# Kernel optimization log

Measured on AMD Instinct MI355X. Metric: run time of the kernel, lower is better.

Reference implementation:

```python
import jax, jax.numpy as jnp
import numpy as np

N = 50000   # nodes per graph
E = 500000  # edges per graph
F_IN = 128  # num_features
H = 128     # hidden_channels
C = 64      # num_classes
G = 64      # graphs per batch
NEG_SLOPE = 0.2


def setup_inputs() -> dict:
    key = jax.random.key(0)
    ks = jax.random.split(key, 16)
    s = 1.0 / np.sqrt(H)
    return {
        "x1": jax.random.normal(ks[0], (N, F_IN), jnp.float32),
        "x2": jax.random.normal(ks[1], (N, F_IN), jnp.float32),
        # stacked params for the 2 GATConv layers (F_IN == H so shapes match)
        "convW": jax.random.normal(ks[2], (2, H, H), jnp.float32) * s,
        "att_src": jax.random.normal(ks[3], (2, H), jnp.float32) * s,
        "att_dst": jax.random.normal(ks[4], (2, H), jnp.float32) * s,
        "conv_b": jnp.zeros((2, H), jnp.float32),
        "mlp_w1": jax.random.normal(ks[5], (H, H), jnp.float32) * s,
        "mlp_b1": jnp.zeros((H,), jnp.float32),
        "mlp_w2": jax.random.normal(ks[6], (H, C), jnp.float32) * s,
        "mlp_b2": jnp.zeros((C,), jnp.float32),
        "edge_index1": jax.random.randint(ks[7], (2, E), 0, N, jnp.int64),
        "batch1": jnp.sort(jax.random.randint(ks[8], (N,), 0, G, jnp.int64)),
        "edge_index2": jax.random.randint(ks[9], (2, E), 0, N, jnp.int64),
        "batch2": jnp.sort(jax.random.randint(ks[10], (N,), 0, G, jnp.int64)),
    }


def gat_conv(x, src, dst, W, a_s, a_d, b):
    # PyG GATConv, heads=1, add_self_loops already applied in src/dst
    n = x.shape[0]
    h = x @ W                                   # [N, H]
    alpha_s = h @ a_s                           # [N]
    alpha_d = h @ a_d                           # [N]
    e = alpha_s[src] + alpha_d[dst]             # [Etot]
    e = jnp.where(e > 0, e, NEG_SLOPE * e)      # leaky_relu
    # segment softmax over incoming edges of each dst node
    m = jax.ops.segment_max(e, dst, num_segments=n)
    ex = jnp.exp(e - m[dst])
    denom = jax.ops.segment_sum(ex, dst, num_segments=n)
    alpha = ex / denom[dst]                     # [Etot]
    out = jax.ops.segment_sum(h[src] * alpha[:, None], dst, num_segments=n)
    return out + b


def reference(x1, x2, convW, att_src, att_dst, conv_b,
              mlp_w1, mlp_b1, mlp_w2, mlp_b2,
              edge_index1, batch1, edge_index2, batch2):
    def branch(x, ei):
        n = x.shape[0]
        loops = jnp.arange(n, dtype=ei.dtype)
        src = jnp.concatenate([ei[0], loops])
        dst = jnp.concatenate([ei[1], loops])
        # num_layers=3 -> 2 convs; i != num_layers-1 always true -> ELU after each
        for l in range(2):
            x = gat_conv(x, src, dst, convW[l], att_src[l], att_dst[l], conv_b[l])
            x = jax.nn.elu(x)
            # dropout p=0.5 is identity in eval mode
        return jax.nn.relu(x @ mlp_w1 + mlp_b1) @ mlp_w2 + mlp_b2

    h1 = branch(x1, edge_index1)
    h2 = branch(x2, edge_index2)
    p1 = jax.ops.segment_sum(h1, batch1, num_segments=G)  # [G, C]
    p2 = jax.ops.segment_sum(h2, batch2, num_segments=G)  # [G, C]
    return p1.T @ p2                                      # [C, C]
```

## Files before the change

### kernel.cpp

```cpp
#include <hip/hip_runtime.h>
#include <cstdint>
#include <cstddef>

#define NNODES 50000
#define NEDGES 500000
#define NTOT (NEDGES + NNODES)
#define HDIM 128
#define CDIM 64
#define GDIM 64
#define NB 250
#define NPB 200
#define CHUNK 2048
#define NCHB ((NEDGES + CHUNK - 1) / CHUNK)

typedef __bf16 bf16x8 __attribute__((ext_vector_type(8)));
typedef __bf16 bf16x2 __attribute__((ext_vector_type(2)));
typedef float f32x4 __attribute__((ext_vector_type(4)));


__global__ __launch_bounds__(256) void k_setup(const float* __restrict__ convW,
                                               const float* __restrict__ w1,
                                               const float* __restrict__ w2,
                                               const float* __restrict__ a_s,
                                               const float* __restrict__ a_d,
                                               __bf16* __restrict__ WtC,
                                               __bf16* __restrict__ Wt1,
                                               __bf16* __restrict__ Wt2,
                                               float* __restrict__ Wa,
                                               float* __restrict__ p) {
    int b = blockIdx.x, tid = threadIdx.x;
    if (b < 128) {
        int i = b * 256 + tid;
        int mat = i >> 14, rem = i & 16383;
        int k = rem >> 7, n = rem & 127;
        WtC[mat * 16384 + n * 128 + k] = (__bf16)convW[i];
    } else if (b < 192) {
        int i = (b - 128) * 256 + tid;
        int k = i >> 7, n = i & 127;
        Wt1[n * 128 + k] = (__bf16)w1[i];
    } else if (b < 224) {
        int i = (b - 192) * 256 + tid;
        int k = i >> 6, n = i & 63;
        Wt2[n * 128 + k] = (__bf16)w2[i];
    } else if (b == 224) {
        for (int o = tid; o < 512; o += 256) {
            int l = o >> 8, r = o & 255;
            int type = r >> 7, k = r & 127;
            const float* a = (type ? a_d : a_s) + l * 128;
            const float* Wrow = convW + l * 16384 + k * 128;
            float s = 0.f;
            for (int j = 0; j < 128; j++) s += Wrow[j] * a[j];
            Wa[o] = s;
        }
    } else {
        for (int i = tid; i < 2 * GDIM * CDIM; i += 256) p[i] = 0.f;
    }
}


__global__ __launch_bounds__(256) void k_bhist(const int* __restrict__ ei0,
                                               const int* __restrict__ ei1,
                                               int* __restrict__ bcntB, int e) {
    __shared__ int h[NB];
    const int* dst = (blockIdx.y ? ei1 : ei0) + NEDGES;
    int* bcnt = bcntB + blockIdx.y * NB;
    for (int t = threadIdx.x; t < NB; t += 256) h[t] = 0;
    __syncthreads();
    int base = blockIdx.x * CHUNK;
    int lim = min(base + CHUNK, e);
    for (int i = base + threadIdx.x; i < lim; i += 256) atomicAdd(&h[dst[i] / NPB], 1);
    __syncthreads();
    for (int t = threadIdx.x; t < NB; t += 256)
        if (h[t]) atomicAdd(&bcnt[t], h[t]);
}

__global__ __launch_bounds__(256) void k_bscan(const int* __restrict__ bcntB,
                                               int* __restrict__ boffB,
                                               int* __restrict__ bcurB) {
    __shared__ int s[256];
    int t = threadIdx.x;
    const int* bcnt = bcntB + blockIdx.y * NB;
    int* boff = boffB + blockIdx.y * (NB + 1);
    int* bcur = bcurB + blockIdx.y * NB;
    int v = (t < NB) ? bcnt[t] : 0;
    s[t] = v;
    __syncthreads();
    for (int off = 1; off < 256; off <<= 1) {
        int x = (t >= off) ? s[t - off] : 0;
        __syncthreads();
        s[t] += x;
        __syncthreads();
    }
    if (t < NB) {
        boff[t + 1] = s[t];
        bcur[t] = s[t] - v;
        if (t == 0) boff[0] = 0;
    }
}

__global__ __launch_bounds__(256) void k_part(const int* __restrict__ ei0,
                                              const int* __restrict__ ei1,
                                              int* __restrict__ bcurB,
                                              int2* __restrict__ partB, int e) {
    __shared__ int cnt[NB], boffL[NB], gbase[NB], cur2[NB];
    __shared__ int tmp[256];
    __shared__ int2 staged[CHUNK];
    const int* eis = blockIdx.y ? ei1 : ei0;
    int* bcur = bcurB + blockIdx.y * NB;
    int2* part = partB + blockIdx.y * (size_t)NEDGES;
    int t = threadIdx.x;
    for (int i = t; i < NB; i += 256) { cnt[i] = 0; cur2[i] = 0; }
    __syncthreads();
    int base = blockIdx.x * CHUNK;
    int lim = min(base + CHUNK, e);
    int nloc = lim - base;

    int s_[8], d_[8], b_[8];
    bool v_[8];
#pragma unroll
    for (int k = 0; k < 8; k++) {
        int i = base + k * 256 + t;
        v_[k] = i < lim;
        s_[k] = 0; d_[k] = 0; b_[k] = 0;
        if (v_[k]) {
            s_[k] = eis[i];
            d_[k] = eis[NEDGES + i];
            b_[k] = d_[k] / NPB;
            atomicAdd(&cnt[b_[k]], 1);
        }
    }
    __syncthreads();
    tmp[t] = (t < NB) ? cnt[t] : 0;
    __syncthreads();
    for (int off = 1; off < 256; off <<= 1) {
        int x = (t >= off) ? tmp[t - off] : 0;
        __syncthreads();
        tmp[t] += x;
        __syncthreads();
    }
    if (t < NB) boffL[t] = tmp[t] - cnt[t];
    __syncthreads();
    if (t < NB) {
        int c = cnt[t];
        gbase[t] = c ? atomicAdd(&bcur[t], c) : 0;
    }
    __syncthreads();
#pragma unroll
    for (int k = 0; k < 8; k++) {
        if (v_[k]) {
            int pos = atomicAdd(&cur2[b_[k]], 1);
            staged[boffL[b_[k]] + pos] = make_int2(s_[k], d_[k]);
        }
    }
    __syncthreads();
    for (int i = t; i < nloc; i += 256) {
        int2 r = staged[i];
        int b = r.y / NPB;
        part[gbase[b] + (i - boffL[b])] = r;
    }
}

__global__ __launch_bounds__(256) void k_place(const int2* __restrict__ partB,
                                               const int* __restrict__ boffB,
                                               int* __restrict__ rpB, size_t sNp1,
                                               int* __restrict__ colB, size_t sE) {
    __shared__ int h[NPB];
    __shared__ int lds4[4];
    int b = blockIdx.x;
    const int* boff = boffB + blockIdx.y * (NB + 1);
    const int2* part = partB + blockIdx.y * (size_t)NEDGES;
    int* row_ptr = rpB + blockIdx.y * sNp1;
    int* col = colB + blockIdx.y * sE;
    int t = threadIdx.x;
    int n0 = b * NPB;
    if (t < NPB) h[t] = 0;
    __syncthreads();
    int beg = boff[b], end = boff[b + 1];
    for (int i = beg + t; i < end; i += 256) atomicAdd(&h[part[i].y - n0], 1);
    __syncthreads();
    int v = (t < NPB) ? h[t] : 0;
    int lane = t & 63, wid = t >> 6;
    int incl = v;
#pragma unroll
    for (int off = 1; off < 64; off <<= 1) {
        int nv = __shfl_up(incl, off);
        if (lane >= off) incl += nv;
    }
    if (lane == 63) lds4[wid] = incl;
    __syncthreads();
    if (t == 0) {
        int s = 0;
#pragma unroll
        for (int j = 0; j < 4; j++) { s += lds4[j]; lds4[j] = s; }
    }
    __syncthreads();
    if (wid > 0) incl += lds4[wid - 1];
    if (t < NPB) {
        int rp_end = beg + n0 + incl + t + 1;
        row_ptr[n0 + t + 1] = rp_end;
        int rp_start = rp_end - v - 1;
        col[rp_start] = n0 + t;
        h[t] = rp_start + 1;
        if (b == 0 && t == 0) row_ptr[0] = 0;
    }
    __syncthreads();
    for (int i = beg + t; i < end; i += 256) {
        int2 r = part[i];
        int p = atomicAdd(&h[r.y - n0], 1);
        col[p] = r.x;
    }
}


template <bool AF32>
__global__ __launch_bounds__(256) void k_gemm_conv(const float* __restrict__ x0,
                                                   const float* __restrict__ x1,
                                                   const __bf16* __restrict__ Ab, size_t As_,
                                                   const __bf16* __restrict__ Wt,
                                                   const float* __restrict__ Was,
                                                   const float* __restrict__ Wad,
                                                   float* __restrict__ asB, float* __restrict__ adB,
                                                   size_t aS,
                                                   __bf16* __restrict__ OutB, size_t Os_, int M) {
    constexpr int BN = 128;
    __shared__ __align__(16) unsigned short As[64][136];
    __shared__ __align__(16) unsigned short Bs[BN][136];
    const int tid = threadIdx.x;
    const int lane = tid & 63, w = tid >> 6;
    const int row0 = blockIdx.x * 64;
    __bf16* Out = OutB + blockIdx.y * Os_;

#pragma unroll
    for (int t = 0; t < 4; t++) {
        int ch = t * 256 + tid;
        int r = ch >> 4, cx = ch & 15;
        int grow = row0 + r;
        bf16x8 v = {};
        if (grow < M) {
            if (AF32) {
                const float* Ap = (blockIdx.y ? x1 : x0) + (size_t)grow * 128 + cx * 8;
                float4 f0 = *reinterpret_cast<const float4*>(Ap);
                float4 f1 = *reinterpret_cast<const float4*>(Ap + 4);
                v[0] = (__bf16)f0.x; v[1] = (__bf16)f0.y; v[2] = (__bf16)f0.z; v[3] = (__bf16)f0.w;
                v[4] = (__bf16)f1.x; v[5] = (__bf16)f1.y; v[6] = (__bf16)f1.z; v[7] = (__bf16)f1.w;
            } else {
                v = *reinterpret_cast<const bf16x8*>(Ab + blockIdx.y * As_ + (size_t)grow * 128 + cx * 8);
            }
        }
        *reinterpret_cast<bf16x8*>(&As[r][cx * 8]) = v;
    }
#pragma unroll
    for (int t = 0; t < 8; t++) {
        int ch = t * 256 + tid;
        int r = ch >> 4, cx = ch & 15;
        bf16x8 v = *reinterpret_cast<const bf16x8*>(Wt + (size_t)r * 128 + cx * 8);
        *reinterpret_cast<bf16x8*>(&Bs[r][cx * 8]) = v;
    }
    __syncthreads();

    {
        int row = tid >> 2, seg = tid & 3;
        float ss = 0.f, sd = 0.f;
#pragma unroll
        for (int k = 0; k < 32; k++) {
            int kk = seg * 32 + k;
            float a = __int_as_float(((unsigned)As[row][kk]) << 16);
            ss += a * Was[kk];
            sd += a * Wad[kk];
        }
        ss += __shfl_xor(ss, 1); ss += __shfl_xor(ss, 2);
        sd += __shfl_xor(sd, 1); sd += __shfl_xor(sd, 2);
        if (seg == 0) {
            int grow = row0 + row;
            if (grow < M) {
                (asB + blockIdx.y * aS)[grow] = ss;
                (adB + blockIdx.y * aS)[grow] = sd;
            }
        }
    }

    const int wr0 = (w >> 1) * 32;
    const int wc0 = (w & 1) * 64;
    f32x4 acc[2][4] = {};

#pragma unroll
    for (int ks = 0; ks < 4; ks++) {
        const int koff = ks * 32 + (lane >> 4) * 8;
        bf16x8 af[2], bfr[4];
#pragma unroll
        for (int mf = 0; mf < 2; mf++)
            af[mf] = *reinterpret_cast<const bf16x8*>(&As[wr0 + mf * 16 + (lane & 15)][koff]);
#pragma unroll
        for (int nf = 0; nf < 4; nf++)
            bfr[nf] = *reinterpret_cast<const bf16x8*>(&Bs[wc0 + nf * 16 + (lane & 15)][koff]);
#pragma unroll
        for (int mf = 0; mf < 2; mf++)
#pragma unroll
            for (int nf = 0; nf < 4; nf++)
                acc[mf][nf] = __builtin_amdgcn_mfma_f32_16x16x32_bf16(af[mf], bfr[nf], acc[mf][nf], 0, 0, 0);
    }

#pragma unroll
    for (int mf = 0; mf < 2; mf++) {
#pragma unroll
        for (int r = 0; r < 4; r++) {
            int row = row0 + wr0 + mf * 16 + (lane >> 4) * 4 + r;
            if (row >= M) continue;
#pragma unroll
            for (int nf = 0; nf < 4; nf++) {
                int colc = wc0 + nf * 16 + (lane & 15);
                Out[(size_t)row * BN + colc] = (__bf16)acc[mf][nf][r];
            }
        }
    }
}


__global__ __launch_bounds__(256) void k_gat_agg(const __bf16* __restrict__ hB, size_t hS,
                                                 const float* __restrict__ asB,
                                                 const float* __restrict__ adB, size_t aS,
                                                 const int* __restrict__ rpB, size_t sNp1,
                                                 const int* __restrict__ colB, size_t sE,
                                                 const float* __restrict__ bias,
                                                 __bf16* __restrict__ outB, size_t oS, int n) {
    int grp = threadIdx.x >> 4;
    int node = blockIdx.x * 16 + grp;
    int l = threadIdx.x & 15;
    if (node >= n) return;
    const float* alpha_s = asB + blockIdx.y * aS;
    const int* row_ptr = rpB + blockIdx.y * sNp1;
    const int* col = colB + blockIdx.y * sE;
    const char* hbase = (const char*)(hB + blockIdx.y * hS);
    float ad = (adB + blockIdx.y * aS)[node];
    int beg = row_ptr[node], end = row_ptr[node + 1];
    int deg = end - beg;
    int foff = l * 16;

    float acc[8] = {0.f, 0.f, 0.f, 0.f, 0.f, 0.f, 0.f, 0.f};

    if (deg <= 16) {
        bool v = l < deg;
        int c = 0;
        float e = -1e30f;
        if (v) {
            c = col[beg + l];
            float t = alpha_s[c] + ad;
            e = (t > 0.f) ? t : 0.2f * t;
        }
        float m = e;
#pragma unroll
        for (int off = 8; off; off >>= 1) m = fmaxf(m, __shfl_xor(m, off));
        float ex = v ? __expf(e - m) : 0.f;
        float den = ex;
#pragma unroll
        for (int off = 8; off; off >>= 1) den += __shfl_xor(den, off);
        float wn = ex / den;

        int base = (grp << 4) & 63;
        for (int e2 = 0; e2 < deg; e2 += 2) {
            int i1 = base + e2, i2 = base + e2 + 1;
            int s1 = __shfl(c, i1); float w1 = __shfl(wn, i1);
            int s2 = __shfl(c, i2); float w2 = __shfl(wn, i2);
            bool h2v = (e2 + 1) < deg;
            s2 = h2v ? s2 : s1;
            w2 = h2v ? w2 : 0.f;
            bf16x8 h1 = *reinterpret_cast<const bf16x8*>(hbase + ((size_t)(unsigned)s1 << 8) + foff);
            bf16x8 hh2 = *reinterpret_cast<const bf16x8*>(hbase + ((size_t)(unsigned)s2 << 8) + foff);
#pragma unroll
            for (int q = 0; q < 8; q++) acc[q] += w1 * (float)h1[q] + w2 * (float)hh2[q];
        }
    } else {
        float m = -1e30f;
        for (int i = beg + l; i < end; i += 16) {
            float t = alpha_s[col[i]] + ad;
            t = (t > 0.f) ? t : 0.2f * t;
            m = fmaxf(m, t);
        }
#pragma unroll
        for (int off = 8; off; off >>= 1) m = fmaxf(m, __shfl_xor(m, off));
        float den = 0.f;
        for (int i = beg + l; i < end; i += 16) {
            float t = alpha_s[col[i]] + ad;
            t = (t > 0.f) ? t : 0.2f * t;
            den += __expf(t - m);
        }
#pragma unroll
        for (int off = 8; off; off >>= 1) den += __shfl_xor(den, off);
        float rinv = 1.f / den;
        for (int e2 = beg; e2 < end; e2++) {
            int cc = col[e2];
            float t = alpha_s[cc] + ad;
            t = (t > 0.f) ? t : 0.2f * t;
            float wv = __expf(t - m) * rinv;
            bf16x8 hv = *reinterpret_cast<const bf16x8*>(hbase + ((size_t)(unsigned)cc << 8) + foff);
#pragma unroll
            for (int q = 0; q < 8; q++) acc[q] += wv * (float)hv[q];
        }
    }

    float4 b0 = *reinterpret_cast<const float4*>(bias + l * 8);
    float4 b1 = *reinterpret_cast<const float4*>(bias + l * 8 + 4);
    float bb[8] = {b0.x, b0.y, b0.z, b0.w, b1.x, b1.y, b1.z, b1.w};
    bf16x8 o;
#pragma unroll
    for (int q = 0; q < 8; q++) {
        float x = acc[q] + bb[q];
        x = (x > 0.f) ? x : __expf(x) - 1.f;
        o[q] = (__bf16)x;
    }
    *reinterpret_cast<bf16x8*>((char*)(outB + blockIdx.y * oS) + ((size_t)(unsigned)node << 8) + foff) = o;
}


__global__ __launch_bounds__(256) void k_mlp_pool(const __bf16* __restrict__ AbB, size_t As_,
                                                  const __bf16* __restrict__ Wt1,
                                                  const __bf16* __restrict__ Wt2,
                                                  const float* __restrict__ b1,
                                                  const float* __restrict__ b2,
                                                  const int* __restrict__ bat0,
                                                  const int* __restrict__ bat1,
                                                  float* __restrict__ pB, size_t pS, int M) {
    __shared__ __align__(16) unsigned short As[64][136];
    __shared__ __align__(16) unsigned short Bs[128][136];
    const int tid = threadIdx.x;
    const int lane = tid & 63, w = tid >> 6;
    const int row0 = blockIdx.x * 64;
    const __bf16* Ab = AbB + blockIdx.y * As_;
    const int* batch = blockIdx.y ? bat1 : bat0;
    float* p = pB + blockIdx.y * pS;

#pragma unroll
    for (int t = 0; t < 4; t++) {
        int ch = t * 256 + tid;
        int r = ch >> 4, cx = ch & 15;
        int grow = row0 + r;
        bf16x8 v = {};
        if (grow < M) v = *reinterpret_cast<const bf16x8*>(Ab + (size_t)grow * 128 + cx * 8);
        *reinterpret_cast<bf16x8*>(&As[r][cx * 8]) = v;
    }
#pragma unroll
    for (int t = 0; t < 8; t++) {
        int ch = t * 256 + tid;
        int r = ch >> 4, cx = ch & 15;
        bf16x8 v = *reinterpret_cast<const bf16x8*>(Wt1 + (size_t)r * 128 + cx * 8);
        *reinterpret_cast<bf16x8*>(&Bs[r][cx * 8]) = v;
    }
    __syncthreads();

    {
        const int wr0 = (w >> 1) * 32;
        const int wc0 = (w & 1) * 64;
        f32x4 acc[2][4] = {};
#pragma unroll
        for (int ks = 0; ks < 4; ks++) {
            const int koff = ks * 32 + (lane >> 4) * 8;
            bf16x8 af[2], bfr[4];
#pragma unroll
            for (int mf = 0; mf < 2; mf++)
                af[mf] = *reinterpret_cast<const bf16x8*>(&As[wr0 + mf * 16 + (lane & 15)][koff]);
#pragma unroll
            for (int nf = 0; nf < 4; nf++)
                bfr[nf] = *reinterpret_cast<const bf16x8*>(&Bs[wc0 + nf * 16 + (lane & 15)][koff]);
#pragma unroll
            for (int mf = 0; mf < 2; mf++)
#pragma unroll
                for (int nf = 0; nf < 4; nf++)
                    acc[mf][nf] = __builtin_amdgcn_mfma_f32_16x16x32_bf16(af[mf], bfr[nf], acc[mf][nf], 0, 0, 0);
        }
        __syncthreads();
#pragma unroll
        for (int mf = 0; mf < 2; mf++)
#pragma unroll
            for (int r = 0; r < 4; r++) {
                int row = wr0 + mf * 16 + (lane >> 4) * 4 + r;
#pragma unroll
                for (int nf = 0; nf < 4; nf++) {
                    int colc = wc0 + nf * 16 + (lane & 15);
                    float v = fmaxf(acc[mf][nf][r] + b1[colc], 0.f);
                    As[row][colc] = __builtin_bit_cast(unsigned short, (__bf16)v);
                }
            }
#pragma unroll
        for (int t = 0; t < 4; t++) {
            int ch = t * 256 + tid;
            int r = ch >> 4, cx = ch & 15;
            bf16x8 v = *reinterpret_cast<const bf16x8*>(Wt2 + (size_t)r * 128 + cx * 8);
            *reinterpret_cast<bf16x8*>(&Bs[r][cx * 8]) = v;
        }
        __syncthreads();
    }

    const int wr2 = w * 16;
    f32x4 acc2[4] = {};
#pragma unroll
    for (int ks = 0; ks < 4; ks++) {
        const int koff = ks * 32 + (lane >> 4) * 8;
        bf16x8 a2 = *reinterpret_cast<const bf16x8*>(&As[wr2 + (lane & 15)][koff]);
#pragma unroll
        for (int nf = 0; nf < 4; nf++) {
            bf16x8 bf2 = *reinterpret_cast<const bf16x8*>(&Bs[nf * 16 + (lane & 15)][koff]);
            acc2[nf] = __builtin_amdgcn_mfma_f32_16x16x32_bf16(a2, bf2, acc2[nf], 0, 0, 0);
        }
    }

    int q = lane >> 4, c = lane & 15;
    bool full = (row0 + 63) < M;
    int g0 = batch[min(row0, M - 1)];
    int g1 = batch[min(row0 + 63, M - 1)];
    if (full && g0 == g1) {
        float s0 = acc2[0][0] + acc2[0][1] + acc2[0][2] + acc2[0][3];
        float s1 = acc2[1][0] + acc2[1][1] + acc2[1][2] + acc2[1][3];
        float s2 = acc2[2][0] + acc2[2][1] + acc2[2][2] + acc2[2][3];
        float s3 = acc2[3][0] + acc2[3][1] + acc2[3][2] + acc2[3][3];
        s0 += __shfl_xor(s0, 16); s0 += __shfl_xor(s0, 32);
        s1 += __shfl_xor(s1, 16); s1 += __shfl_xor(s1, 32);
        s2 += __shfl_xor(s2, 16); s2 += __shfl_xor(s2, 32);
        s3 += __shfl_xor(s3, 16); s3 += __shfl_xor(s3, 32);
        float v = (q & 2) ? ((q & 1) ? s3 : s2) : ((q & 1) ? s1 : s0);
        v += 16.f * b2[q * 16 + c];
        atomicAdd(&p[g0 * CDIM + q * 16 + c], v);
    } else {
        float b2v[4];
#pragma unroll
        for (int nf = 0; nf < 4; nf++) b2v[nf] = b2[nf * 16 + c];
#pragma unroll
        for (int r = 0; r < 4; r++) {
            int row = row0 + wr2 + q * 4 + r;
            if (row >= M) continue;
            int g = batch[row];
#pragma unroll
            for (int nf = 0; nf < 4; nf++)
                atomicAdd(&p[g * CDIM + nf * 16 + c], acc2[nf][r] + b2v[nf]);
        }
    }
}


__global__ __launch_bounds__(64) void k_final(const float* __restrict__ p, float* __restrict__ out) {
    int i = blockIdx.x;
    int j = threadIdx.x;
    const float* p1 = p;
    const float* p2 = p + GDIM * CDIM;
    float s = 0.f;
    for (int g = 0; g < GDIM; ++g) s += p1[g * CDIM + i] * p2[g * CDIM + j];
    out[i * CDIM + j] = s;
}


static inline size_t align_up(size_t x, size_t a) { return (x + a - 1) & ~(a - 1); }

struct Ws {
    __bf16 *Hb, *Yb;
    __bf16 *WtC, *Wt1, *Wt2;
    float *alpha_s, *alpha_d, *Wa, *p;
    int *row_ptr, *col;
    int *bcnt, *boff, *bcur;
    int2* part;
    size_t sNH, sN, sNp1, sE;
    size_t need;
};

static Ws carve(void* ws, bool combined) {
    char* p = (char*)ws;
    size_t off = 0;
    Ws w;
    int nb = combined ? 2 : 1;
    auto take = [&](size_t bytes) {
        char* r = p + off;
        off = align_up(off + bytes, 256);
        return r;
    };
    w.Hb = (__bf16*)take((size_t)nb * NNODES * HDIM * 2);
    w.Yb = (__bf16*)take((size_t)nb * NNODES * HDIM * 2);
    w.alpha_s = (float*)take((size_t)nb * NNODES * 4);
    w.alpha_d = (float*)take((size_t)nb * NNODES * 4);
    w.col = (int*)take((size_t)nb * NTOT * 4);
    w.part = (int2*)take((size_t)nb * NEDGES * 8);
    w.row_ptr = (int*)take((size_t)nb * (NNODES + 1) * 4);
    w.bcnt = (int*)take((size_t)2 * NB * 4);
    w.boff = (int*)take((size_t)2 * (NB + 1) * 4);
    w.bcur = (int*)take((size_t)2 * NB * 4);
    w.WtC = (__bf16*)take((size_t)2 * HDIM * HDIM * 2);
    w.Wt1 = (__bf16*)take((size_t)HDIM * HDIM * 2);
    w.Wt2 = (__bf16*)take((size_t)HDIM * CDIM * 2);
    w.Wa = (float*)take((size_t)512 * 4);
    w.p = (float*)take((size_t)2 * GDIM * CDIM * 4);
    w.need = off;
    size_t s = combined ? 1 : 0;
    w.sNH = s * (size_t)NNODES * HDIM;
    w.sN = s * (size_t)NNODES;
    w.sNp1 = s * (size_t)(NNODES + 1);
    w.sE = s * (size_t)NTOT;
    return w;
}

static void pipeline(const Ws& w, const float* xA, const float* xB,
                     const int* eiA, const int* eiB,
                     const int* batA, const int* batB,
                     const float* conv_b, const float* b1, const float* b2,
                     float* pbase, size_t pstride, int yc, hipStream_t stream) {
    const int N = NNODES, E = NEDGES;
    dim3 gC(NCHB, yc), gB(NB, yc), g1(1, yc);
    dim3 gW((N + 15) / 16, yc);
    dim3 gG((N + 63) / 64, yc);

    hipMemsetAsync(w.bcnt, 0, (size_t)yc * NB * 4, stream);
    k_bhist<<<gC, 256, 0, stream>>>(eiA, eiB, w.bcnt, E);
    k_bscan<<<g1, 256, 0, stream>>>(w.bcnt, w.boff, w.bcur);
    k_part<<<gC, 256, 0, stream>>>(eiA, eiB, w.bcur, w.part, E);
    k_place<<<gB, 256, 0, stream>>>(w.part, w.boff, w.row_ptr, w.sNp1, w.col, w.sE);

    k_gemm_conv<true><<<gG, 256, 0, stream>>>(
        xA, xB, nullptr, 0, w.WtC, w.Wa, w.Wa + 128,
        w.alpha_s, w.alpha_d, w.sN, w.Hb, w.sNH, N);
    k_gat_agg<<<gW, 256, 0, stream>>>(w.Hb, w.sNH, w.alpha_s, w.alpha_d, w.sN,
                                      w.row_ptr, w.sNp1, w.col, w.sE, conv_b, w.Yb, w.sNH, N);
    k_gemm_conv<false><<<gG, 256, 0, stream>>>(
        nullptr, nullptr, w.Yb, w.sNH, w.WtC + HDIM * HDIM, w.Wa + 256, w.Wa + 384,
        w.alpha_s, w.alpha_d, w.sN, w.Hb, w.sNH, N);
    k_gat_agg<<<gW, 256, 0, stream>>>(w.Hb, w.sNH, w.alpha_s, w.alpha_d, w.sN,
                                      w.row_ptr, w.sNp1, w.col, w.sE, conv_b + HDIM, w.Yb, w.sNH, N);
    k_mlp_pool<<<gG, 256, 0, stream>>>(w.Yb, w.sNH, w.Wt1, w.Wt2, b1, b2,
                                       batA, batB, pbase, pstride, N);
}

extern "C" void kernel_launch(void* const* d_in, const int* in_sizes, int n_in, void* d_out,
                              int out_size, void* d_ws, size_t ws_size, hipStream_t stream) {
    const float* x1      = (const float*)d_in[0];
    const float* x2      = (const float*)d_in[1];
    const float* convW   = (const float*)d_in[2];
    const float* att_src = (const float*)d_in[3];
    const float* att_dst = (const float*)d_in[4];
    const float* conv_b  = (const float*)d_in[5];
    const float* mlp_w1  = (const float*)d_in[6];
    const float* mlp_b1  = (const float*)d_in[7];
    const float* mlp_w2  = (const float*)d_in[8];
    const float* mlp_b2  = (const float*)d_in[9];
    const int* ei1       = (const int*)d_in[10];
    const int* batch1    = (const int*)d_in[11];
    const int* ei2       = (const int*)d_in[12];
    const int* batch2    = (const int*)d_in[13];
    float* out = (float*)d_out;

    Ws wc = carve(d_ws, true);
    bool combined = ws_size >= wc.need;
    Ws w = combined ? wc : carve(d_ws, false);

    k_setup<<<226, 256, 0, stream>>>(convW, mlp_w1, mlp_w2, att_src, att_dst,
                                     w.WtC, w.Wt1, w.Wt2, w.Wa, w.p);

    if (combined) {
        pipeline(w, x1, x2, ei1, ei2, batch1, batch2, conv_b,
                 mlp_b1, mlp_b2, w.p, (size_t)GDIM * CDIM, 2, stream);
    } else {
        pipeline(w, x1, x1, ei1, ei1, batch1, batch1, conv_b,
                 mlp_b1, mlp_b2, w.p, 0, 1, stream);
        pipeline(w, x2, x2, ei2, ei2, batch2, batch2, conv_b,
                 mlp_b1, mlp_b2, w.p + GDIM * CDIM, 0, 1, stream);
    }

    k_final<<<CDIM, 64, 0, stream>>>(w.p, out);
}
```

Measured before the change: 346.9 us.

## Fuse pipeline into a persistent cooperative megakernel and pack partitioned edges

```diff
diff --git a/kernel.cpp b/kernel.cpp
--- a/kernel.cpp
+++ b/kernel.cpp
@@ -1,6 +1,9 @@
 #include <hip/hip_runtime.h>
+#include <hip/hip_cooperative_groups.h>
 #include <cstdint>
 #include <cstddef>
+
+namespace cg = cooperative_groups;
 
 #define NNODES 50000
 #define NEDGES 500000
@@ -12,76 +15,80 @@
 #define NPB 200
 #define CHUNK 2048
 #define NCHB ((NEDGES + CHUNK - 1) / CHUNK)
+#define SNH ((size_t)NNODES * HDIM)
+#define SN ((size_t)NNODES)
+#define SNP1 ((size_t)(NNODES + 1))
+#define SE ((size_t)NTOT)
+#define GEMM_TILES ((NNODES + 63) / 64)
+#define AGG_UNITS (NNODES / 16)
 
 typedef __bf16 bf16x8 __attribute__((ext_vector_type(8)));
 typedef __bf16 bf16x2 __attribute__((ext_vector_type(2)));
 typedef float f32x4 __attribute__((ext_vector_type(4)));
-
-
-__global__ __launch_bounds__(256) void k_setup(const float* __restrict__ convW,
-                                               const float* __restrict__ w1,
-                                               const float* __restrict__ w2,
-                                               const float* __restrict__ a_s,
-                                               const float* __restrict__ a_d,
-                                               __bf16* __restrict__ WtC,
-                                               __bf16* __restrict__ Wt1,
-                                               __bf16* __restrict__ Wt2,
-                                               float* __restrict__ Wa,
-                                               float* __restrict__ p) {
-    int b = blockIdx.x, tid = threadIdx.x;
+typedef unsigned short ushort_t;
+
+struct MegaArgs {
+    const float *x0, *x1, *convW, *att_s, *att_d, *conv_b, *w1, *b1, *w2, *b2;
+    const int *ei0, *ei1, *bat0, *bat1;
+    __bf16 *Hb, *Yb, *WtC, *Wt1, *Wt2;
+    float *alpha_s, *alpha_d, *Wa, *p;
+    int *row_ptr, *col, *bcnt, *boff, *bcur;
+    unsigned int* part;
+    float* out;
+    int nblk;
+};
+
+
+__device__ void d_setup(int b, int tid, const MegaArgs& A) {
     if (b < 128) {
         int i = b * 256 + tid;
         int mat = i >> 14, rem = i & 16383;
         int k = rem >> 7, n = rem & 127;
-        WtC[mat * 16384 + n * 128 + k] = (__bf16)convW[i];
+        A.WtC[mat * 16384 + n * 128 + k] = (__bf16)A.convW[i];
     } else if (b < 192) {
         int i = (b - 128) * 256 + tid;
         int k = i >> 7, n = i & 127;
-        Wt1[n * 128 + k] = (__bf16)w1[i];
+        A.Wt1[n * 128 + k] = (__bf16)A.w1[i];
     } else if (b < 224) {
         int i = (b - 192) * 256 + tid;
         int k = i >> 6, n = i & 63;
-        Wt2[n * 128 + k] = (__bf16)w2[i];
+        A.Wt2[n * 128 + k] = (__bf16)A.w2[i];
     } else if (b == 224) {
         for (int o = tid; o < 512; o += 256) {
             int l = o >> 8, r = o & 255;
             int type = r >> 7, k = r & 127;
-            const float* a = (type ? a_d : a_s) + l * 128;
-            const float* Wrow = convW + l * 16384 + k * 128;
+            const float* a = (type ? A.att_d : A.att_s) + l * 128;
+            const float* Wrow = A.convW + l * 16384 + k * 128;
             float s = 0.f;
             for (int j = 0; j < 128; j++) s += Wrow[j] * a[j];
-            Wa[o] = s;
+            A.Wa[o] = s;
         }
     } else {
-        for (int i = tid; i < 2 * GDIM * CDIM; i += 256) p[i] = 0.f;
-    }
-}
-
-
-__global__ __launch_bounds__(256) void k_bhist(const int* __restrict__ ei0,
-                                               const int* __restrict__ ei1,
-                                               int* __restrict__ bcntB, int e) {
-    __shared__ int h[NB];
-    const int* dst = (blockIdx.y ? ei1 : ei0) + NEDGES;
-    int* bcnt = bcntB + blockIdx.y * NB;
-    for (int t = threadIdx.x; t < NB; t += 256) h[t] = 0;
-    __syncthreads();
-    int base = blockIdx.x * CHUNK;
-    int lim = min(base + CHUNK, e);
-    for (int i = base + threadIdx.x; i < lim; i += 256) atomicAdd(&h[dst[i] / NPB], 1);
-    __syncthreads();
-    for (int t = threadIdx.x; t < NB; t += 256)
+        for (int i = tid; i < 2 * GDIM * CDIM; i += 256) A.p[i] = 0.f;
+    }
+}
+
+__device__ void d_bhist(int u, int br, int tid, const MegaArgs& A, char* smem) {
+    int* h = (int*)smem;
+    const int* dst = (br ? A.ei1 : A.ei0) + NEDGES;
+    int* bcnt = A.bcnt + br * NB;
+    for (int t = tid; t < NB; t += 256) h[t] = 0;
+    __syncthreads();
+    int base = u * CHUNK;
+    int lim = min(base + CHUNK, NEDGES);
+    for (int i = base + tid; i < lim; i += 256) atomicAdd(&h[dst[i] / NPB], 1);
+    __syncthreads();
+    for (int t = tid; t < NB; t += 256)
         if (h[t]) atomicAdd(&bcnt[t], h[t]);
-}
-
-__global__ __launch_bounds__(256) void k_bscan(const int* __restrict__ bcntB,
-                                               int* __restrict__ boffB,
-                                               int* __restrict__ bcurB) {
-    __shared__ int s[256];
-    int t = threadIdx.x;
-    const int* bcnt = bcntB + blockIdx.y * NB;
-    int* boff = boffB + blockIdx.y * (NB + 1);
-    int* bcur = bcurB + blockIdx.y * NB;
+    __syncthreads();
+}
+
+__device__ void d_bscan(int br, int tid, const MegaArgs& A, char* smem) {
+    int* s = (int*)smem;
+    const int* bcnt = A.bcnt + br * NB;
+    int* boff = A.boff + br * (NB + 1);
+    int* bcur = A.bcur + br * NB;
+    int t = tid;
     int v = (t < NB) ? bcnt[t] : 0;
     s[t] = v;
     __syncthreads();
@@ -96,36 +103,40 @@
         bcur[t] = s[t] - v;
         if (t == 0) boff[0] = 0;
     }
-}
-
-__global__ __launch_bounds__(256) void k_part(const int* __restrict__ ei0,
-                                              const int* __restrict__ ei1,
-                                              int* __restrict__ bcurB,
-                                              int2* __restrict__ partB, int e) {
-    __shared__ int cnt[NB], boffL[NB], gbase[NB], cur2[NB];
-    __shared__ int tmp[256];
-    __shared__ int2 staged[CHUNK];
-    const int* eis = blockIdx.y ? ei1 : ei0;
-    int* bcur = bcurB + blockIdx.y * NB;
-    int2* part = partB + blockIdx.y * (size_t)NEDGES;
-    int t = threadIdx.x;
+    __syncthreads();
+}
+
+__device__ void d_part(int u, int br, int tid, const MegaArgs& A, char* smem) {
+    int* cnt = (int*)smem;
+    int* boffL = cnt + NB;
+    int* gbase = boffL + NB;
+    int* cur2 = gbase + NB;
+    int* tmp = cur2 + NB;
+    unsigned int* staged = (unsigned int*)(tmp + 256);
+    const int* eis = br ? A.ei1 : A.ei0;
+    int* bcur = A.bcur + br * NB;
+    unsigned int* part = A.part + br * (size_t)NEDGES;
+    int t = tid;
     for (int i = t; i < NB; i += 256) { cnt[i] = 0; cur2[i] = 0; }
     __syncthreads();
-    int base = blockIdx.x * CHUNK;
-    int lim = min(base + CHUNK, e);
+    int base = u * CHUNK;
+    int lim = min(base + CHUNK, NEDGES);
     int nloc = lim - base;
 
-    int s_[8], d_[8], b_[8];
+    int b_[8];
+    unsigned int pk_[8];
     bool v_[8];
 #pragma unroll
     for (int k = 0; k < 8; k++) {
         int i = base + k * 256 + t;
         v_[k] = i < lim;
-        s_[k] = 0; d_[k] = 0; b_[k] = 0;
+        pk_[k] = 0; b_[k] = 0;
         if (v_[k]) {
-            s_[k] = eis[i];
-            d_[k] = eis[NEDGES + i];
-            b_[k] = d_[k] / NPB;
+            int s = eis[i];
+            int d = eis[NEDGES + i];
+            b_[k] = d / NPB;
+            int dloc = d - b_[k] * NPB;
+            pk_[k] = (unsigned)s | ((unsigned)dloc << 16) | ((unsigned)b_[k] << 24);
             atomicAdd(&cnt[b_[k]], 1);
         }
     }
@@ -149,34 +160,31 @@
     for (int k = 0; k < 8; k++) {
         if (v_[k]) {
             int pos = atomicAdd(&cur2[b_[k]], 1);
-            staged[boffL[b_[k]] + pos] = make_int2(s_[k], d_[k]);
+            staged[boffL[b_[k]] + pos] = pk_[k];
         }
     }
     __syncthreads();
     for (int i = t; i < nloc; i += 256) {
-        int2 r = staged[i];
-        int b = r.y / NPB;
+        unsigned int r = staged[i];
+        int b = (int)(r >> 24);
         part[gbase[b] + (i - boffL[b])] = r;
     }
-}
-
-__global__ __launch_bounds__(256) void k_place(const int2* __restrict__ partB,
-                                               const int* __restrict__ boffB,
-                                               int* __restrict__ rpB, size_t sNp1,
-                                               int* __restrict__ colB, size_t sE) {
-    __shared__ int h[NPB];
-    __shared__ int lds4[4];
-    int b = blockIdx.x;
-    const int* boff = boffB + blockIdx.y * (NB + 1);
-    const int2* part = partB + blockIdx.y * (size_t)NEDGES;
-    int* row_ptr = rpB + blockIdx.y * sNp1;
-    int* col = colB + blockIdx.y * sE;
-    int t = threadIdx.x;
+    __syncthreads();
+}
+
+__device__ void d_place(int b, int br, int tid, const MegaArgs& A, char* smem) {
+    int* h = (int*)smem;
+    int* lds4 = h + NPB;
+    const int* boff = A.boff + br * (NB + 1);
+    const unsigned int* part = A.part + br * (size_t)NEDGES;
+    int* row_ptr = A.row_ptr + br * SNP1;
+    int* col = A.col + br * SE;
+    int t = tid;
     int n0 = b * NPB;
     if (t < NPB) h[t] = 0;
     __syncthreads();
     int beg = boff[b], end = boff[b + 1];
-    for (int i = beg + t; i < end; i += 256) atomicAdd(&h[part[i].y - n0], 1);
+    for (int i = beg + t; i < end; i += 256) atomicAdd(&h[(part[i] >> 16) & 0xFF], 1);
     __syncthreads();
     int v = (t < NPB) ? h[t] : 0;
     int lane = t & 63, wid = t >> 6;
@@ -205,30 +213,27 @@
     }
     __syncthreads();
     for (int i = beg + t; i < end; i += 256) {
-        int2 r = part[i];
-        int p = atomicAdd(&h[r.y - n0], 1);
-        col[p] = r.x;
-    }
-}
-
+        unsigned int r = part[i];
+        int p = atomicAdd(&h[(r >> 16) & 0xFF], 1);
+        col[p] = (int)(r & 0xFFFF);
+    }
+    __syncthreads();
+}
 
 template <bool AF32>
-__global__ __launch_bounds__(256) void k_gemm_conv(const float* __restrict__ x0,
-                                                   const float* __restrict__ x1,
-                                                   const __bf16* __restrict__ Ab, size_t As_,
-                                                   const __bf16* __restrict__ Wt,
-                                                   const float* __restrict__ Was,
-                                                   const float* __restrict__ Wad,
-                                                   float* __restrict__ asB, float* __restrict__ adB,
-                                                   size_t aS,
-                                                   __bf16* __restrict__ OutB, size_t Os_, int M) {
-    constexpr int BN = 128;
-    __shared__ __align__(16) unsigned short As[64][136];
-    __shared__ __align__(16) unsigned short Bs[BN][136];
-    const int tid = threadIdx.x;
+__device__ void d_gemm_tile(int u, int br, int tid, const MegaArgs& A, char* smem) {
+    ushort_t (*As)[136] = (ushort_t(*)[136])smem;
+    ushort_t (*Bs)[136] = (ushort_t(*)[136])(smem + 64 * 136 * 2);
     const int lane = tid & 63, w = tid >> 6;
-    const int row0 = blockIdx.x * 64;
-    __bf16* Out = OutB + blockIdx.y * Os_;
+    const int row0 = u * 64;
+    const int M = NNODES;
+    const __bf16* Wt = AF32 ? A.WtC : (A.WtC + HDIM * HDIM);
+    const float* Was = AF32 ? A.Wa : (A.Wa + 256);
+    const float* Wad = AF32 ? (A.Wa + 128) : (A.Wa + 384);
+    const __bf16* Ab = A.Yb + br * SNH;
+    __bf16* Out = A.Hb + br * SNH;
+    float* asB = A.alpha_s + br * SN;
+    float* adB = A.alpha_d + br * SN;
 
 #pragma unroll
     for (int t = 0; t < 4; t++) {
@@ -238,13 +243,13 @@
         bf16x8 v = {};
         if (grow < M) {
             if (AF32) {
-                const float* Ap = (blockIdx.y ? x1 : x0) + (size_t)grow * 128 + cx * 8;
+                const float* Ap = (br ? A.x1 : A.x0) + (size_t)grow * 128 + cx * 8;
                 float4 f0 = *reinterpret_cast<const float4*>(Ap);
                 float4 f1 = *reinterpret_cast<const float4*>(Ap + 4);
                 v[0] = (__bf16)f0.x; v[1] = (__bf16)f0.y; v[2] = (__bf16)f0.z; v[3] = (__bf16)f0.w;
                 v[4] = (__bf16)f1.x; v[5] = (__bf16)f1.y; v[6] = (__bf16)f1.z; v[7] = (__bf16)f1.w;
             } else {
-                v = *reinterpret_cast<const bf16x8*>(Ab + blockIdx.y * As_ + (size_t)grow * 128 + cx * 8);
+                v = *reinterpret_cast<const bf16x8*>(Ab + (size_t)grow * 128 + cx * 8);
             }
         }
         *reinterpret_cast<bf16x8*>(&As[r][cx * 8]) = v;
@@ -272,17 +277,13 @@
         sd += __shfl_xor(sd, 1); sd += __shfl_xor(sd, 2);
         if (seg == 0) {
             int grow = row0 + row;
-            if (grow < M) {
-                (asB + blockIdx.y * aS)[grow] = ss;
-                (adB + blockIdx.y * aS)[grow] = sd;
-            }
+            if (grow < M) { asB[grow] = ss; adB[grow] = sd; }
         }
     }
 
     const int wr0 = (w >> 1) * 32;
     const int wc0 = (w & 1) * 64;
     f32x4 acc[2][4] = {};
-
 #pragma unroll
     for (int ks = 0; ks < 4; ks++) {
         const int koff = ks * 32 + (lane >> 4) * 8;
@@ -299,7 +300,6 @@
             for (int nf = 0; nf < 4; nf++)
                 acc[mf][nf] = __builtin_amdgcn_mfma_f32_16x16x32_bf16(af[mf], bfr[nf], acc[mf][nf], 0, 0, 0);
     }
-
 #pragma unroll
     for (int mf = 0; mf < 2; mf++) {
 #pragma unroll
@@ -309,29 +309,24 @@
 #pragma unroll
             for (int nf = 0; nf < 4; nf++) {
                 int colc = wc0 + nf * 16 + (lane & 15);
-                Out[(size_t)row * BN + colc] = (__bf16)acc[mf][nf][r];
+                Out[(size_t)row * 128 + colc] = (__bf16)acc[mf][nf][r];
             }
         }
     }
-}
-
-
-__global__ __launch_bounds__(256) void k_gat_agg(const __bf16* __restrict__ hB, size_t hS,
-                                                 const float* __restrict__ asB,
-                                                 const float* __restrict__ adB, size_t aS,
-                                                 const int* __restrict__ rpB, size_t sNp1,
-                                                 const int* __restrict__ colB, size_t sE,
-                                                 const float* __restrict__ bias,
-                                                 __bf16* __restrict__ outB, size_t oS, int n) {
-    int grp = threadIdx.x >> 4;
-    int node = blockIdx.x * 16 + grp;
-    int l = threadIdx.x & 15;
-    if (node >= n) return;
-    const float* alpha_s = asB + blockIdx.y * aS;
-    const int* row_ptr = rpB + blockIdx.y * sNp1;
-    const int* col = colB + blockIdx.y * sE;
-    const char* hbase = (const char*)(hB + blockIdx.y * hS);
-    float ad = (adB + blockIdx.y * aS)[node];
+    __syncthreads();
+}
+
+__device__ void d_agg(int u, int br, int layer, int tid, const MegaArgs& A) {
+    int grp = tid >> 4;
+    int node = u * 16 + grp;
+    int l = tid & 15;
+    if (node >= NNODES) return;
+    const float* alpha_s = A.alpha_s + br * SN;
+    const int* row_ptr = A.row_ptr + br * SNP1;
+    const int* col = A.col + br * SE;
+    const char* hbase = (const char*)(A.Hb + br * SNH);
+    const float* bias = A.conv_b + layer * HDIM;
+    float ad = (A.alpha_d + br * SN)[node];
     int beg = row_ptr[node], end = row_ptr[node + 1];
     int deg = end - beg;
     int foff = l * 16;
@@ -408,26 +403,18 @@
         x = (x > 0.f) ? x : __expf(x) - 1.f;
         o[q] = (__bf16)x;
     }
-    *reinterpret_cast<bf16x8*>((char*)(outB + blockIdx.y * oS) + ((size_t)(unsigned)node << 8) + foff) = o;
-}
-
-
-__global__ __launch_bounds__(256) void k_mlp_pool(const __bf16* __restrict__ AbB, size_t As_,
-                                                  const __bf16* __restrict__ Wt1,
-                                                  const __bf16* __restrict__ Wt2,
-                                                  const float* __restrict__ b1,
-                                                  const float* __restrict__ b2,
-                                                  const int* __restrict__ bat0,
-                                                  const int* __restrict__ bat1,
-                                                  float* __restrict__ pB, size_t pS, int M) {
-    __shared__ __align__(16) unsigned short As[64][136];
-    __shared__ __align__(16) unsigned short Bs[128][136];
-    const int tid = threadIdx.x;
+    *reinterpret_cast<bf16x8*>((char*)(A.Yb + br * SNH) + ((size_t)(unsigned)node << 8) + foff) = o;
+}
+
+__device__ void d_mlp(int u, int br, int tid, const MegaArgs& A, char* smem) {
+    ushort_t (*As)[136] = (ushort_t(*)[136])smem;
+    ushort_t (*Bs)[136] = (ushort_t(*)[136])(smem + 64 * 136 * 2);
     const int lane = tid & 63, w = tid >> 6;
-    const int row0 = blockIdx.x * 64;
-    const __bf16* Ab = AbB + blockIdx.y * As_;
-    const int* batch = blockIdx.y ? bat1 : bat0;
-    float* p = pB + blockIdx.y * pS;
+    const int row0 = u * 64;
+    const int M = NNODES;
+    const __bf16* Ab = A.Yb + br * SNH;
+    const int* batch = br ? A.bat1 : A.bat0;
+    float* p = A.p + br * (GDIM * CDIM);
 
 #pragma unroll
     for (int t = 0; t < 4; t++) {
@@ -442,11 +429,10 @@
     for (int t = 0; t < 8; t++) {
         int ch = t * 256 + tid;
         int r = ch >> 4, cx = ch & 15;
-        bf16x8 v = *reinterpret_cast<const bf16x8*>(Wt1 + (size_t)r * 128 + cx * 8);
+        bf16x8 v = *reinterpret_cast<const bf16x8*>(A.Wt1 + (size_t)r * 128 + cx * 8);
         *reinterpret_cast<bf16x8*>(&Bs[r][cx * 8]) = v;
     }
     __syncthreads();
-
     {
         const int wr0 = (w >> 1) * 32;
         const int wc0 = (w & 1) * 64;
@@ -476,20 +462,19 @@
 #pragma unroll
                 for (int nf = 0; nf < 4; nf++) {
                     int colc = wc0 + nf * 16 + (lane & 15);
-                    float v = fmaxf(acc[mf][nf][r] + b1[colc], 0.f);
-                    As[row][colc] = __builtin_bit_cast(unsigned short, (__bf16)v);
+                    float v = fmaxf(acc[mf][nf][r] + A.b1[colc], 0.f);
+                    As[row][colc] = __builtin_bit_cast(ushort_t, (__bf16)v);
                 }
             }
 #pragma unroll
         for (int t = 0; t < 4; t++) {
             int ch = t * 256 + tid;
             int r = ch >> 4, cx = ch & 15;
-            bf16x8 v = *reinterpret_cast<const bf16x8*>(Wt2 + (size_t)r * 128 + cx * 8);
+            bf16x8 v = *reinterpret_cast<const bf16x8*>(A.Wt2 + (size_t)r * 128 + cx * 8);
             *reinterpret_cast<bf16x8*>(&Bs[r][cx * 8]) = v;
         }
         __syncthreads();
     }
-
     const int wr2 = w * 16;
     f32x4 acc2[4] = {};
 #pragma unroll
@@ -502,7 +487,6 @@
             acc2[nf] = __builtin_amdgcn_mfma_f32_16x16x32_bf16(a2, bf2, acc2[nf], 0, 0, 0);
         }
     }
-
     int q = lane >> 4, c = lane & 15;
     bool full = (row0 + 63) < M;
     int g0 = batch[min(row0, M - 1)];
@@ -517,12 +501,12 @@
         s2 += __shfl_xor(s2, 16); s2 += __shfl_xor(s2, 32);
         s3 += __shfl_xor(s3, 16); s3 += __shfl_xor(s3, 32);
         float v = (q & 2) ? ((q & 1) ? s3 : s2) : ((q & 1) ? s1 : s0);
-        v += 16.f * b2[q * 16 + c];
+        v += 16.f * A.b2[q * 16 + c];
         atomicAdd(&p[g0 * CDIM + q * 16 + c], v);
     } else {
         float b2v[4];
 #pragma unroll
-        for (int nf = 0; nf < 4; nf++) b2v[nf] = b2[nf * 16 + c];
+        for (int nf = 0; nf < 4; nf++) b2v[nf] = A.b2[nf * 16 + c];
 #pragma unroll
         for (int r = 0; r < 4; r++) {
             int row = row0 + wr2 + q * 4 + r;
@@ -533,50 +517,146 @@
                 atomicAdd(&p[g * CDIM + nf * 16 + c], acc2[nf][r] + b2v[nf]);
         }
     }
-}
-
-
-__global__ __launch_bounds__(64) void k_final(const float* __restrict__ p, float* __restrict__ out) {
-    int i = blockIdx.x;
-    int j = threadIdx.x;
-    const float* p1 = p;
-    const float* p2 = p + GDIM * CDIM;
+    __syncthreads();
+}
+
+__device__ void d_final(int i, int tid, const MegaArgs& A) {
+    if (tid >= 64) return;
+    const float* p1 = A.p;
+    const float* p2 = A.p + GDIM * CDIM;
     float s = 0.f;
-    for (int g = 0; g < GDIM; ++g) s += p1[g * CDIM + i] * p2[g * CDIM + j];
-    out[i * CDIM + j] = s;
+    for (int g = 0; g < GDIM; ++g) s += p1[g * CDIM + i] * p2[g * CDIM + tid];
+    A.out[i * CDIM + tid] = s;
+}
+
+
+__global__ __launch_bounds__(256, 3) void k_mega(MegaArgs A) {
+    cg::grid_group grid = cg::this_grid();
+    __shared__ __align__(16) char smem[52224];
+    const int bid = blockIdx.x, tid = threadIdx.x, G = A.nblk;
+
+    for (int u = bid; u < 226 + 2 * NCHB; u += G) {
+        if (u < 226) d_setup(u, tid, A);
+        else if (u < 226 + NCHB) d_bhist(u - 226, 0, tid, A, smem);
+        else d_bhist(u - 226 - NCHB, 1, tid, A, smem);
+        __syncthreads();
+    }
+    grid.sync();
+    if (bid == 0) d_bscan(0, tid, A, smem);
+    else if (bid == 1) d_bscan(1, tid, A, smem);
+    else for (int u = bid - 2; u < GEMM_TILES; u += G - 2) d_gemm_tile<true>(u, 0, tid, A, smem);
+    grid.sync();
+    if (bid < NCHB) { d_part(bid, 0, tid, A, smem); d_part(bid, 1, tid, A, smem); }
+    else for (int u = bid - NCHB; u < 520; u += G - NCHB) d_gemm_tile<true>(u, 1, tid, A, smem);
+    grid.sync();
+    if (bid < NB) { d_place(bid, 0, tid, A, smem); d_place(bid, 1, tid, A, smem); }
+    else for (int u = 520 + (bid - NB); u < GEMM_TILES; u += G - NB) d_gemm_tile<true>(u, 1, tid, A, smem);
+    grid.sync();
+    for (int u = bid; u < AGG_UNITS; u += G) d_agg(u, 0, 0, tid, A);
+    grid.sync();
+    const int S = (G / 3) * 2;
+    if (bid < S) { for (int u = bid; u < AGG_UNITS; u += S) d_agg(u, 1, 0, tid, A); }
+    else for (int u = bid - S; u < GEMM_TILES; u += G - S) d_gemm_tile<false>(u, 0, tid, A, smem);
+    grid.sync();
+    if (bid < S) { for (int u = bid; u < AGG_UNITS; u += S) d_agg(u, 0, 1, tid, A); }
+    else for (int u = bid - S; u < GEMM_TILES; u += G - S) d_gemm_tile<false>(u, 1, tid, A, smem);
+    grid.sync();
+    if (bid < S) { for (int u = bid; u < GEMM_TILES; u += S) d_mlp(u, 0, tid, A, smem); }
+    else for (int u = bid - S; u < AGG_UNITS; u += G - S) d_agg(u, 1, 1, tid, A);
+    grid.sync();
+    for (int u = bid; u < GEMM_TILES; u += G) d_mlp(u, 1, tid, A, smem);
+    grid.sync();
+    if (bid < CDIM) d_final(bid, tid, A);
+}
+
+
+__global__ __launch_bounds__(256) void k_setup(const float* __restrict__ convW,
+                                               const float* __restrict__ w1,
+                                               const float* __restrict__ w2,
+                                               const float* __restrict__ a_s,
+                                               const float* __restrict__ a_d,
+                                               __bf16* __restrict__ WtC, __bf16* __restrict__ Wt1,
+                                               __bf16* __restrict__ Wt2, float* __restrict__ Wa,
+                                               float* __restrict__ p) {
+    MegaArgs A = {};
+    A.convW = convW; A.w1 = w1; A.w2 = w2; A.att_s = a_s; A.att_d = a_d;
+    A.WtC = WtC; A.Wt1 = Wt1; A.Wt2 = Wt2; A.Wa = Wa; A.p = p;
+    d_setup(blockIdx.x, threadIdx.x, A);
+}
+
+__global__ __launch_bounds__(256) void k_bhist(const int* ei0, const int* ei1, int* bcnt) {
+    __shared__ char smem[1024];
+    MegaArgs A = {}; A.ei0 = ei0; A.ei1 = ei1; A.bcnt = bcnt;
+    d_bhist(blockIdx.x, blockIdx.y, threadIdx.x, A, smem);
+}
+
+__global__ __launch_bounds__(256) void k_bscan(const int* bcnt, int* boff, int* bcur) {
+    __shared__ char smem[1024];
+    MegaArgs A = {}; A.bcnt = (int*)bcnt; A.boff = boff; A.bcur = bcur;
+    d_bscan(blockIdx.y, threadIdx.x, A, smem);
+}
+
+__global__ __launch_bounds__(256) void k_part(const int* ei0, const int* ei1, int* bcur,
+                                              unsigned int* part) {
+    __shared__ char smem[13312];
+    MegaArgs A = {}; A.ei0 = ei0; A.ei1 = ei1; A.bcur = bcur; A.part = part;
+    d_part(blockIdx.x, blockIdx.y, threadIdx.x, A, smem);
+}
+
+__global__ __launch_bounds__(256) void k_place(const unsigned int* part, const int* boff,
+                                               int* row_ptr, int* col) {
+    __shared__ char smem[1024];
+    MegaArgs A = {}; A.part = (unsigned int*)part; A.boff = (int*)boff;
+    A.row_ptr = row_ptr; A.col = col;
+    d_place(blockIdx.x, blockIdx.y, threadIdx.x, A, smem);
+}
+
+template <bool AF32>
+__global__ __launch_bounds__(256) void k_gemm_conv(MegaArgs A) {
+    __shared__ __align__(16) char smem[52224];
+    d_gemm_tile<AF32>(blockIdx.x, blockIdx.y, threadIdx.x, A, smem);
+}
+
+__global__ __launch_bounds__(256) void k_gat_agg(MegaArgs A, int layer) {
+    d_agg(blockIdx.x, blockIdx.y, layer, threadIdx.x, A);
+}
+
+__global__ __launch_bounds__(256) void k_mlp_pool(MegaArgs A) {
+    __shared__ __align__(16) char smem[52224];
+    d_mlp(blockIdx.x, blockIdx.y, threadIdx.x, A, smem);
+}
+
+__global__ __launch_bounds__(64) void k_final(MegaArgs A) {
+    d_final(blockIdx.x, threadIdx.x, A);
 }
 
 
 static inline size_t align_up(size_t x, size_t a) { return (x + a - 1) & ~(a - 1); }
 
 struct Ws {
-    __bf16 *Hb, *Yb;
-    __bf16 *WtC, *Wt1, *Wt2;
+    __bf16 *Hb, *Yb, *WtC, *Wt1, *Wt2;
     float *alpha_s, *alpha_d, *Wa, *p;
-    int *row_ptr, *col;
-    int *bcnt, *boff, *bcur;
-    int2* part;
-    size_t sNH, sN, sNp1, sE;
+    int *row_ptr, *col, *bcnt, *boff, *bcur;
+    unsigned int* part;
     size_t need;
 };
 
-static Ws carve(void* ws, bool combined) {
+static Ws carve(void* ws) {
     char* p = (char*)ws;
     size_t off = 0;
     Ws w;
-    int nb = combined ? 2 : 1;
     auto take = [&](size_t bytes) {
         char* r = p + off;
         off = align_up(off + bytes, 256);
         return r;
     };
-    w.Hb = (__bf16*)take((size_t)nb * NNODES * HDIM * 2);
-    w.Yb = (__bf16*)take((size_t)nb * NNODES * HDIM * 2);
-    w.alpha_s = (float*)take((size_t)nb * NNODES * 4);
-    w.alpha_d = (float*)take((size_t)nb * NNODES * 4);
-    w.col = (int*)take((size_t)nb * NTOT * 4);
-    w.part = (int2*)take((size_t)nb * NEDGES * 8);
-    w.row_ptr = (int*)take((size_t)nb * (NNODES + 1) * 4);
+    w.Hb = (__bf16*)take((size_t)2 * NNODES * HDIM * 2);
+    w.Yb = (__bf16*)take((size_t)2 * NNODES * HDIM * 2);
+    w.alpha_s = (float*)take((size_t)2 * NNODES * 4);
+    w.alpha_d = (float*)take((size_t)2 * NNODES * 4);
+    w.col = (int*)take((size_t)2 * NTOT * 4);
+    w.part = (unsigned int*)take((size_t)2 * NEDGES * 4);
+    w.row_ptr = (int*)take((size_t)2 * (NNODES + 1) * 4);
     w.bcnt = (int*)take((size_t)2 * NB * 4);
     w.boff = (int*)take((size_t)2 * (NB + 1) * 4);
     w.bcur = (int*)take((size_t)2 * NB * 4);
@@ -586,78 +666,62 @@
     w.Wa = (float*)take((size_t)512 * 4);
     w.p = (float*)take((size_t)2 * GDIM * CDIM * 4);
     w.need = off;
-    size_t s = combined ? 1 : 0;
-    w.sNH = s * (size_t)NNODES * HDIM;
-    w.sN = s * (size_t)NNODES;
-    w.sNp1 = s * (size_t)(NNODES + 1);
-    w.sE = s * (size_t)NTOT;
     return w;
-}
-
-static void pipeline(const Ws& w, const float* xA, const float* xB,
-                     const int* eiA, const int* eiB,
-                     const int* batA, const int* batB,
-                     const float* conv_b, const float* b1, const float* b2,
-                     float* pbase, size_t pstride, int yc, hipStream_t stream) {
-    const int N = NNODES, E = NEDGES;
-    dim3 gC(NCHB, yc), gB(NB, yc), g1(1, yc);
-    dim3 gW((N + 15) / 16, yc);
-    dim3 gG((N + 63) / 64, yc);
-
-    hipMemsetAsync(w.bcnt, 0, (size_t)yc * NB * 4, stream);
-    k_bhist<<<gC, 256, 0, stream>>>(eiA, eiB, w.bcnt, E);
-    k_bscan<<<g1, 256, 0, stream>>>(w.bcnt, w.boff, w.bcur);
-    k_part<<<gC, 256, 0, stream>>>(eiA, eiB, w.bcur, w.part, E);
-    k_place<<<gB, 256, 0, stream>>>(w.part, w.boff, w.row_ptr, w.sNp1, w.col, w.sE);
-
-    k_gemm_conv<true><<<gG, 256, 0, stream>>>(
-        xA, xB, nullptr, 0, w.WtC, w.Wa, w.Wa + 128,
-        w.alpha_s, w.alpha_d, w.sN, w.Hb, w.sNH, N);
-    k_gat_agg<<<gW, 256, 0, stream>>>(w.Hb, w.sNH, w.alpha_s, w.alpha_d, w.sN,
-                                      w.row_ptr, w.sNp1, w.col, w.sE, conv_b, w.Yb, w.sNH, N);
-    k_gemm_conv<false><<<gG, 256, 0, stream>>>(
-        nullptr, nullptr, w.Yb, w.sNH, w.WtC + HDIM * HDIM, w.Wa + 256, w.Wa + 384,
-        w.alpha_s, w.alpha_d, w.sN, w.Hb, w.sNH, N);
-    k_gat_agg<<<gW, 256, 0, stream>>>(w.Hb, w.sNH, w.alpha_s, w.alpha_d, w.sN,
-                                      w.row_ptr, w.sNp1, w.col, w.sE, conv_b + HDIM, w.Yb, w.sNH, N);
-    k_mlp_pool<<<gG, 256, 0, stream>>>(w.Yb, w.sNH, w.Wt1, w.Wt2, b1, b2,
-                                       batA, batB, pbase, pstride, N);
 }
 
 extern "C" void kernel_launch(void* const* d_in, const int* in_sizes, int n_in, void* d_out,
                               int out_size, void* d_ws, size_t ws_size, hipStream_t stream) {
-    const float* x1      = (const float*)d_in[0];
-    const float* x2      = (const float*)d_in[1];
-    const float* convW   = (const float*)d_in[2];
-    const float* att_src = (const float*)d_in[3];
-    const float* att_dst = (const float*)d_in[4];
-    const float* conv_b  = (const float*)d_in[5];
-    const float* mlp_w1  = (const float*)d_in[6];
-    const float* mlp_b1  = (const float*)d_in[7];
-    const float* mlp_w2  = (const float*)d_in[8];
-    const float* mlp_b2  = (const float*)d_in[9];
-    const int* ei1       = (const int*)d_in[10];
-    const int* batch1    = (const int*)d_in[11];
-    const int* ei2       = (const int*)d_in[12];
-    const int* batch2    = (const int*)d_in[13];
-    float* out = (float*)d_out;
-
-    Ws wc = carve(d_ws, true);
-    bool combined = ws_size >= wc.need;
-    Ws w = combined ? wc : carve(d_ws, false);
-
-    k_setup<<<226, 256, 0, stream>>>(convW, mlp_w1, mlp_w2, att_src, att_dst,
-                                     w.WtC, w.Wt1, w.Wt2, w.Wa, w.p);
-
-    if (combined) {
-        pipeline(w, x1, x2, ei1, ei2, batch1, batch2, conv_b,
-                 mlp_b1, mlp_b2, w.p, (size_t)GDIM * CDIM, 2, stream);
-    } else {
-        pipeline(w, x1, x1, ei1, ei1, batch1, batch1, conv_b,
-                 mlp_b1, mlp_b2, w.p, 0, 1, stream);
-        pipeline(w, x2, x2, ei2, ei2, batch2, batch2, conv_b,
-                 mlp_b1, mlp_b2, w.p + GDIM * CDIM, 0, 1, stream);
-    }
-
-    k_final<<<CDIM, 64, 0, stream>>>(w.p, out);
-}
+    MegaArgs A;
+    A.x0 = (const float*)d_in[0];
+    A.x1 = (const float*)d_in[1];
+    A.convW = (const float*)d_in[2];
+    A.att_s = (const float*)d_in[3];
+    A.att_d = (const float*)d_in[4];
+    A.conv_b = (const float*)d_in[5];
+    A.w1 = (const float*)d_in[6];
+    A.b1 = (const float*)d_in[7];
+    A.w2 = (const float*)d_in[8];
+    A.b2 = (const float*)d_in[9];
+    A.ei0 = (const int*)d_in[10];
+    A.bat0 = (const int*)d_in[11];
+    A.ei1 = (const int*)d_in[12];
+    A.bat1 = (const int*)d_in[13];
+    A.out = (float*)d_out;
+
+    Ws w = carve(d_ws);
+    A.Hb = w.Hb; A.Yb = w.Yb; A.WtC = w.WtC; A.Wt1 = w.Wt1; A.Wt2 = w.Wt2;
+    A.alpha_s = w.alpha_s; A.alpha_d = w.alpha_d; A.Wa = w.Wa; A.p = w.p;
+    A.row_ptr = w.row_ptr; A.col = w.col; A.bcnt = w.bcnt; A.boff = w.boff; A.bcur = w.bcur;
+    A.part = w.part;
+
+    hipMemsetAsync(w.bcnt, 0, (size_t)2 * NB * 4, stream);
+
+    int nbpc = 0;
+    hipError_t qe = hipOccupancyMaxActiveBlocksPerMultiprocessor(&nbpc, (const void*)k_mega, 256, 0);
+    int G = (qe == hipSuccess) ? nbpc * 256 : 0;
+    if (G > 768) G = 768;
+    bool coop = (G >= 384);
+    if (coop) {
+        A.nblk = G;
+        void* args[] = {&A};
+        hipError_t le = hipLaunchCooperativeKernel((void*)k_mega, dim3(G), dim3(256), args, 0, stream);
+        if (le != hipSuccess) coop = false;
+    }
+    if (!coop) {
+        A.nblk = 0;
+        k_setup<<<226, 256, 0, stream>>>(A.convW, A.w1, A.w2, A.att_s, A.att_d,
+                                         w.WtC, w.Wt1, w.Wt2, w.Wa, w.p);
+        dim3 gC(NCHB, 2), gB(NB, 2), g1(1, 2);
+        dim3 gW(AGG_UNITS, 2), gG(GEMM_TILES, 2);
+        k_bhist<<<gC, 256, 0, stream>>>(A.ei0, A.ei1, w.bcnt);
+        k_bscan<<<g1, 256, 0, stream>>>(w.bcnt, w.boff, w.bcur);
+        k_part<<<gC, 256, 0, stream>>>(A.ei0, A.ei1, w.bcur, w.part);
+        k_place<<<gB, 256, 0, stream>>>(w.part, w.boff, w.row_ptr, w.col);
+        k_gemm_conv<true><<<gG, 256, 0, stream>>>(A);
+        k_gat_agg<<<gW, 256, 0, stream>>>(A, 0);
+        k_gemm_conv<false><<<gG, 256, 0, stream>>>(A);
+        k_gat_agg<<<gW, 256, 0, stream>>>(A, 1);
+        k_mlp_pool<<<gG, 256, 0, stream>>>(A);
+        k_final<<<CDIM, 64, 0, stream>>>(A);
+    }
+}
```

Result: no change. 346.4 us (-0.1%).
